# Kernel optimization log

Measured on AMD Instinct MI355X. Metric: run time of the kernel, lower is better.

## Reference

```python
import jax, jax.numpy as jnp
import numpy as np

B, N, F, P, HID, OUT = 4, 20000, 8, 12, 64, 1
E = 320000


def _glorot(k, shape):
    lim = float(np.sqrt(6.0 / (shape[0] + shape[1])))
    return jax.random.uniform(k, shape, jnp.float32, -lim, lim)


def setup_inputs() -> dict:
    key = jax.random.key(0)
    ks = jax.random.split(key, 20)
    inp = {
        "x": jax.random.normal(ks[0], (B, N, F, P), jnp.float32),
        "edge_index": jax.random.randint(ks[1], (2, E), 0, N, jnp.int64),
        "edge_attr": jax.random.uniform(ks[2], (E,), jnp.float32),
        # GCNConv weights (stored [in, out]) + biases for z, r, h gates
        "conv_z_w": _glorot(ks[3], (F, HID)), "conv_z_b": jnp.zeros((HID,), jnp.float32),
        "conv_r_w": _glorot(ks[4], (F, HID)), "conv_r_b": jnp.zeros((HID,), jnp.float32),
        "conv_h_w": _glorot(ks[5], (F, HID)), "conv_h_b": jnp.zeros((HID,), jnp.float32),
        # GRU linear layers on cat([conv_out, H]) -> HID (stored [in, out])
        "lin_z_w": _glorot(ks[6], (2 * HID, HID)), "lin_z_b": jnp.zeros((HID,), jnp.float32),
        "lin_r_w": _glorot(ks[7], (2 * HID, HID)), "lin_r_b": jnp.zeros((HID,), jnp.float32),
        "lin_h_w": _glorot(ks[8], (2 * HID, HID)), "lin_h_b": jnp.zeros((HID,), jnp.float32),
        # temporal attention logits over periods
        "attention": jax.random.uniform(ks[9], (P,), jnp.float32),
        # final linear: HID -> OUT*P
        "out_w": _glorot(ks[10], (HID, OUT * P)), "out_b": jnp.zeros((OUT * P,), jnp.float32),
    }
    return inp


def reference(x, edge_index, edge_attr,
              conv_z_w, conv_z_b, conv_r_w, conv_r_b, conv_h_w, conv_h_b,
              lin_z_w, lin_z_b, lin_r_w, lin_r_b, lin_h_w, lin_h_b,
              attention, out_w, out_b):
    Bb, Nn, Ff, Pp = x.shape
    Hh = conv_z_w.shape[1]

    # GCN normalization with self loops: A_hat = D^-1/2 (A + I) D^-1/2
    loop = jnp.arange(Nn)
    row = jnp.concatenate([edge_index[0], loop])
    col = jnp.concatenate([edge_index[1], loop])
    w = jnp.concatenate([edge_attr, jnp.ones((Nn,), x.dtype)])
    deg = jax.ops.segment_sum(w, col, num_segments=Nn)
    dinv = jnp.where(deg > 0, jax.lax.rsqrt(deg), 0.0)
    norm = dinv[row] * w * dinv[col]  # [E+N]

    def gcn(xt, W, b):
        # xt: [B, N, F] -> [B, N, H]
        xw = jnp.einsum('bnf,fh->bnh', xt, W)
        msg = xw[:, row, :] * norm[None, :, None]            # gather over source nodes
        agg = jax.vmap(lambda m: jax.ops.segment_sum(m, col, num_segments=Nn))(msg)
        return agg + b

    H0 = jnp.zeros((Bb, Nn, Hh), x.dtype)  # A3TGCN2 passes H=None each period -> zeros

    def tgcn_cell(xt):
        Z = jax.nn.sigmoid(jnp.concatenate([gcn(xt, conv_z_w, conv_z_b), H0], -1) @ lin_z_w + lin_z_b)
        R = jax.nn.sigmoid(jnp.concatenate([gcn(xt, conv_r_w, conv_r_b), H0], -1) @ lin_r_w + lin_r_b)
        Ht = jnp.tanh(jnp.concatenate([gcn(xt, conv_h_w, conv_h_b), H0 * R], -1) @ lin_h_w + lin_h_b)
        return Z * H0 + (1.0 - Z) * Ht

    probs = jax.nn.softmax(attention)
    xs = jnp.moveaxis(x, -1, 0)  # [P, B, N, F]

    def step(acc, inp):
        xt, p = inp
        return acc + p * tgcn_cell(xt), None

    h_accum, _ = jax.lax.scan(step, jnp.zeros((Bb, Nn, Hh), x.dtype), (xs, probs))

    h = jax.nn.relu(h_accum)
    out = h @ out_w + out_b                 # [B, N, OUT*P]
    return out.reshape(Bb, Nn, -1, Pp)      # [B, N, OUT, P]
```

## Files before the change

### kernel.cpp

```cpp
#include <hip/hip_runtime.h>

#define NN 20000
#define EE 320000
#define NPB 8
#define CAP 64
#define LCAP 80
#define OVCAP 8192

#define WZ_O 0
#define BZ_O 512
#define WH_O 576
#define BH_O 1088
#define OW_O 1152
#define OB_O 1920
#define PR_O 1932
#define NCONST 1944

__device__ __forceinline__ float b2f(unsigned short h) {
  union { unsigned int u; float f; } v; v.u = ((unsigned int)h) << 16; return v.f;
}
__device__ __forceinline__ unsigned short f2b(float f) {
  union { unsigned int u; float f; } v; v.f = f;
  unsigned int u = v.u;
  unsigned int r = (u + 0x7fffu + ((u >> 16) & 1u)) >> 16;
  return (unsigned short)r;
}
__device__ __forceinline__ float ldw(const void* p, int i, int isbf) {
  return isbf ? b2f(((const unsigned short*)p)[i]) : ((const float*)p)[i];
}
__device__ __forceinline__ void upk(unsigned int w, float& x0, float& x1) {
  union { unsigned int u; float f; } lo, hi;
  lo.u = w << 16; hi.u = w & 0xffff0000u;
  x0 = lo.f; x1 = hi.f;
}
__device__ __forceinline__ float degf(unsigned long long dc) {
  return (float)(unsigned int)dc * (1.0f / 1048576.0f);
}

__global__ void k_init(const unsigned int* __restrict__ ei_w,
                       const unsigned int* __restrict__ ea_w,
                       int* __restrict__ flags,
                       unsigned long long* __restrict__ degcnt,
                       int* __restrict__ ovf_cnt,
                       float* __restrict__ consts,
                       const void* czw, const void* czb,
                       const void* chw, const void* chb,
                       const void* lzw, const void* lzb,
                       const void* lhw, const void* lhb,
                       const void* att, const void* ow, const void* ob) {
  int tid = threadIdx.x;
  int i = blockIdx.x * 256 + tid;
  if (i < NN) degcnt[i] = 0ull;
  if (blockIdx.x == 1 && tid == 0) *ovf_cnt = 0;
  if (blockIdx.x != 0) return;

  __shared__ int sfl[2];
  if (tid < 64) {
    unsigned long long b1 = __ballot((ea_w[tid] >> 15) & 1u);
    unsigned long long b2 = __ballot(ei_w[2 * tid + 1] != 0u);
    if (tid == 0) {
      int f0 = (b1 == 0ull) ? 1 : 0;
      int f1 = (b2 == 0ull) ? 1 : 0;
      flags[0] = f0; flags[1] = f1; sfl[0] = f0; sfl[1] = f1;
    }
  }
  __syncthreads();
  int isbf = sfl[0];

  for (int idx = tid; idx < 512; idx += 256) {
    int f = idx >> 6, k = idx & 63;
    float sz = 0.f, sh = 0.f;
    for (int h = 0; h < 64; ++h) {
      sz += ldw(czw, f * 64 + h, isbf) * ldw(lzw, h * 64 + k, isbf);
      sh += ldw(chw, f * 64 + h, isbf) * ldw(lhw, h * 64 + k, isbf);
    }
    consts[WZ_O + idx] = sz; consts[WH_O + idx] = sh;
  }
  for (int idx = tid; idx < 64; idx += 256) {
    float sz = ldw(lzb, idx, isbf), sh = ldw(lhb, idx, isbf);
    for (int h = 0; h < 64; ++h) {
      sz += ldw(czb, h, isbf) * ldw(lzw, h * 64 + idx, isbf);
      sh += ldw(chb, h, isbf) * ldw(lhw, h * 64 + idx, isbf);
    }
    consts[BZ_O + idx] = sz; consts[BH_O + idx] = sh;
  }
  for (int idx = tid; idx < 768; idx += 256) consts[OW_O + idx] = ldw(ow, idx, isbf);
  if (tid < 12) consts[OB_O + tid] = ldw(ob, tid, isbf);
  if (tid == 0) {
    float a[12]; float m = -1e30f;
    for (int p = 0; p < 12; ++p) { a[p] = ldw(att, p, isbf); m = fmaxf(m, a[p]); }
    float ssum = 0.f;
    for (int p = 0; p < 12; ++p) { a[p] = __expf(a[p] - m); ssum += a[p]; }
    for (int p = 0; p < 12; ++p) consts[PR_O + p] = a[p] / ssum;
  }
}

__global__ void k_append(const void* __restrict__ ei, const void* __restrict__ ea,
                         const int* __restrict__ flags,
                         unsigned long long* __restrict__ degcnt,
                         unsigned int* __restrict__ slab,
                         int* __restrict__ ovf_cnt, int* __restrict__ ovf_dst,
                         unsigned int* __restrict__ ovf_pack) {
  int isbf = flags[0], is64 = flags[1];
  int e = blockIdx.x * blockDim.x + threadIdx.x;
  if (e >= EE) return;
  int r, c;
  if (is64) {
    r = (int)((const unsigned int*)ei)[2 * e];
    c = (int)((const unsigned int*)ei)[2 * (EE + e)];
  } else {
    r = ((const int*)ei)[e];
    c = ((const int*)ei)[EE + e];
  }
  unsigned short wb;
  float w;
  if (isbf) { wb = ((const unsigned short*)ea)[e]; w = b2f(wb); }
  else      { w = ((const float*)ea)[e]; wb = f2b(w); }
  unsigned long long pk = (1ull << 32) |
      (unsigned long long)(unsigned int)__float2int_rn(w * 1048576.0f);
  unsigned long long old = atomicAdd(&degcnt[c], pk);
  int pos = (int)(old >> 32);
  unsigned int packed = ((unsigned int)wb << 16) | (unsigned int)r;
  if (pos < CAP) {
    slab[c * CAP + pos] = packed;
  } else {
    int oi = atomicAdd(ovf_cnt, 1);
    if (oi < OVCAP) { ovf_dst[oi] = c; ovf_pack[oi] = packed; }
  }
}

__global__ void __launch_bounds__(192) k_node(
    const void* __restrict__ x,
    const unsigned long long* __restrict__ degcnt,
    const unsigned int* __restrict__ slab,
    const int* __restrict__ ovf_cnt, const int* __restrict__ ovf_dst,
    const unsigned int* __restrict__ ovf_pack,
    const float* __restrict__ consts, const int* __restrict__ flags,
    void* __restrict__ out) {
  __shared__ __align__(16) float sc[792];
  __shared__ __align__(16) float pacc[4 * 384];
  __shared__ __align__(16) float acc[384];
  __shared__ __align__(16) float hpart[768];
  __shared__ __align__(16) float hfin[256];
  __shared__ int   sedge[NPB * LCAP];
  __shared__ float vedge[NPB * LCAP];
  __shared__ int   scnt[NPB];
  __shared__ float sdn[NPB];

  const int tid = threadIdx.x;
  const int isbf = flags[0];
  const int n0 = blockIdx.x * NPB;

  for (int i = tid; i < 792; i += 192) sc[i] = consts[OW_O + i];

  const int g  = tid / 48;
  const int c  = tid % 48;
  const int k  = tid & 63;
  const int g3 = tid >> 6;
  const int bc = c / 12;
  const int oc = 8 * (c % 12);
  const long xoff = (long)bc * (NN * 96) + oc;

  float wz[8], wh[8];
#pragma unroll
  for (int f = 0; f < 8; ++f) {
    wz[f] = consts[WZ_O + f * 64 + k];
    wh[f] = consts[WH_O + f * 64 + k];
  }
  const float bz = consts[BZ_O + k], bh = consts[BH_O + k];

  if (tid < NPB) {
    unsigned long long dc = degcnt[n0 + tid];
    int cnt = (int)(dc >> 32);
    scnt[tid] = cnt < CAP ? cnt : CAP;
    sdn[tid] = rsqrtf(degf(dc) + 1.0f);
  }
  __syncthreads();

  for (int i = tid; i < NPB * CAP; i += 192) {
    int ni = i >> 6, slot = i & (CAP - 1);
    int cnt = (int)(degcnt[n0 + ni] >> 32);
    if (cnt > CAP) cnt = CAP;
    if (slot < cnt) {
      unsigned int pk = slab[(n0 + ni) * CAP + slot];
      int s = (int)(pk & 0xffffu);
      float w = b2f((unsigned short)(pk >> 16));
      sedge[ni * LCAP + slot] = s * 96;
      vedge[ni * LCAP + slot] = w * rsqrtf(degf(degcnt[s]) + 1.0f);
    }
  }
  {
    int ov = ovf_cnt[0];
    if (ov > 0) {
      if (ov > OVCAP) ov = OVCAP;
      for (int i = tid; i < ov; i += 192) {
        unsigned int dd = (unsigned int)(ovf_dst[i] - n0);
        if (dd < NPB) {
          int idx = atomicAdd(&scnt[dd], 1);
          if (idx < LCAP) {
            unsigned int pk = ovf_pack[i];
            int s = (int)(pk & 0xffffu);
            float w = b2f((unsigned short)(pk >> 16));
            sedge[dd * LCAP + idx] = s * 96;
            vedge[dd * LCAP + idx] = w * rsqrtf(degf(degcnt[s]) + 1.0f);
          }
        }
      }
    }
  }
  __syncthreads();

  for (int ni = 0; ni < NPB; ++ni) {
    const int n = n0 + ni;
    int m = scnt[ni]; if (m > LCAP) m = LCAP;
    const float dn = sdn[ni];
    float a[8];
#pragma unroll
    for (int t = 0; t < 8; ++t) a[t] = 0.f;

    if (isbf) {
      const unsigned short* xb = (const unsigned short*)x;
      for (int j = g; j < m; j += 4) {
        int soff = sedge[ni * LCAP + j];
        float v = vedge[ni * LCAP + j];
        uint4 u = *(const uint4*)(xb + xoff + soff);
        float x0, x1;
        upk(u.x, x0, x1); a[0] += v * x0; a[1] += v * x1;
        upk(u.y, x0, x1); a[2] += v * x0; a[3] += v * x1;
        upk(u.z, x0, x1); a[4] += v * x0; a[5] += v * x1;
        upk(u.w, x0, x1); a[6] += v * x0; a[7] += v * x1;
      }
      if (g == 0) {
        uint4 u = *(const uint4*)(xb + xoff + (long)n * 96);
        float x0, x1;
        upk(u.x, x0, x1); a[0] += dn * x0; a[1] += dn * x1;
        upk(u.y, x0, x1); a[2] += dn * x0; a[3] += dn * x1;
        upk(u.z, x0, x1); a[4] += dn * x0; a[5] += dn * x1;
        upk(u.w, x0, x1); a[6] += dn * x0; a[7] += dn * x1;
      }
    } else {
      const float* xf = (const float*)x;
      for (int j = g; j < m; j += 4) {
        int soff = sedge[ni * LCAP + j];
        float v = vedge[ni * LCAP + j];
        const float4* px = (const float4*)(xf + xoff + soff);
        float4 u0 = px[0], u1 = px[1];
        a[0] += v * u0.x; a[1] += v * u0.y; a[2] += v * u0.z; a[3] += v * u0.w;
        a[4] += v * u1.x; a[5] += v * u1.y; a[6] += v * u1.z; a[7] += v * u1.w;
      }
      if (g == 0) {
        const float4* px = (const float4*)(xf + xoff + (long)n * 96);
        float4 u0 = px[0], u1 = px[1];
        a[0] += dn * u0.x; a[1] += dn * u0.y; a[2] += dn * u0.z; a[3] += dn * u0.w;
        a[4] += dn * u1.x; a[5] += dn * u1.y; a[6] += dn * u1.z; a[7] += dn * u1.w;
      }
    }
    {
      float4* pg = (float4*)&pacc[g * 384 + 8 * c];
      pg[0] = make_float4(a[0], a[1], a[2], a[3]);
      pg[1] = make_float4(a[4], a[5], a[6], a[7]);
    }
    __syncthreads();
    for (int i = tid; i < 384; i += 192) {
      int b = i / 96, r = i % 96, p = r >> 3, f = r & 7;
      int src = b * 96 + f * 12 + p;
      acc[i] = dn * (pacc[src] + pacc[384 + src] + pacc[768 + src] + pacc[1152 + src]);
    }
    __syncthreads();

    float hb0 = 0.f, hb1 = 0.f, hb2 = 0.f, hb3 = 0.f;
#pragma unroll
    for (int pi = 0; pi < 4; ++pi) {
      int p = g3 + 3 * pi;
      float pr = sc[780 + p];
#pragma unroll
      for (int b = 0; b < 4; ++b) {
        const float4* A = (const float4*)&acc[b * 96 + p * 8];
        float4 A0 = A[0], A1 = A[1];
        float za = bz + A0.x * wz[0] + A0.y * wz[1] + A0.z * wz[2] + A0.w * wz[3]
                      + A1.x * wz[4] + A1.y * wz[5] + A1.z * wz[6] + A1.w * wz[7];
        float ta = bh + A0.x * wh[0] + A0.y * wh[1] + A0.z * wh[2] + A0.w * wh[3]
                      + A1.x * wh[4] + A1.y * wh[5] + A1.z * wh[6] + A1.w * wh[7];
        float ea = __expf(za);
        float eh = __expf(2.0f * fminf(ta, 40.0f));
        float cc = pr * (eh - 1.0f) * __builtin_amdgcn_rcpf((1.0f + ea) * (1.0f + eh));
        if (b == 0) hb0 += cc; else if (b == 1) hb1 += cc;
        else if (b == 2) hb2 += cc; else hb3 += cc;
      }
    }
    hpart[g3 * 256 +   0 + k] = hb0;
    hpart[g3 * 256 +  64 + k] = hb1;
    hpart[g3 * 256 + 128 + k] = hb2;
    hpart[g3 * 256 + 192 + k] = hb3;
    __syncthreads();
    for (int i = tid; i < 256; i += 192)
      hfin[i] = fmaxf(hpart[i] + hpart[256 + i] + hpart[512 + i], 0.f);
    __syncthreads();

    if (tid < 48) {
      int b = tid / 12, p = tid % 12;
      float o = sc[768 + p];
#pragma unroll 8
      for (int k2 = 0; k2 < 64; ++k2) o += hfin[b * 64 + k2] * sc[k2 * 12 + p];
      int oi = (b * NN + n) * 12 + p;
      if (isbf) ((unsigned short*)out)[oi] = f2b(o);
      else      ((float*)out)[oi] = o;
    }
  }
}

extern "C" void kernel_launch(void* const* d_in, const int* in_sizes, int n_in,
                              void* d_out, int out_size, void* d_ws, size_t ws_size,
                              hipStream_t stream) {
  const void* x   = d_in[0];
  const void* ei  = d_in[1];
  const void* ea  = d_in[2];
  const void* czw = d_in[3];
  const void* czb = d_in[4];
  const void* chw = d_in[7];
  const void* chb = d_in[8];
  const void* lzw = d_in[9];
  const void* lzb = d_in[10];
  const void* lhw = d_in[13];
  const void* lhb = d_in[14];
  const void* att = d_in[15];
  const void* ow  = d_in[16];
  const void* ob  = d_in[17];

  char* ws = (char*)d_ws;
  int*   flags   = (int*)  (ws + 0);
  float* consts  = (float*)(ws + 256);
  unsigned long long* degcnt = (unsigned long long*)(ws + 8192);
  int*   ovf_cnt = (int*)  (ws + 168192);
  int*   ovf_dst = (int*)  (ws + 168448);
  unsigned int* ovf_pack = (unsigned int*)(ws + 201216);
  unsigned int* slab     = (unsigned int*)(ws + 240000);

  k_init<<<dim3(79), dim3(256), 0, stream>>>((const unsigned int*)ei,
                                             (const unsigned int*)ea, flags, degcnt,
                                             ovf_cnt, consts, czw, czb, chw, chb,
                                             lzw, lzb, lhw, lhb, att, ow, ob);
  k_append<<<dim3(1250), dim3(256), 0, stream>>>(ei, ea, flags, degcnt, slab,
                                                 ovf_cnt, ovf_dst, ovf_pack);
  k_node<<<dim3(NN / NPB), dim3(192), 0, stream>>>(x, degcnt, slab, ovf_cnt, ovf_dst,
                                                   ovf_pack, consts, flags, d_out);
}
```

Measured before the change: 260.2 us.

## Split node kernel across batch dimension with 16-way edge parallelism

Launches the node kernel with one block per (batch, node-group), so each block handles a single batch element and splits edges 16 ways instead of 4. The reduction, gate computation and output projection are reshaped to per-batch sizes, and the output dot product uses shuffle-based partial sums. This raises parallelism and cuts per-thread serial edge work. In exchange, the per-block edge list setup, degree loads and weight loads are now repeated four times.

Result: slower. 292.4 us (+12.4%).

```diff
diff --git a/kernel.cpp b/kernel.cpp
--- a/kernel.cpp
+++ b/kernel.cpp
@@ -3,9 +3,11 @@
 #define NN 20000
 #define EE 320000
 #define NPB 8
+#define NBLK 2500
 #define CAP 64
 #define LCAP 80
 #define OVCAP 8192
+#define PROW 104
 
 #define WZ_O 0
 #define BZ_O 512
@@ -137,29 +139,28 @@
     const unsigned int* __restrict__ ovf_pack,
     const float* __restrict__ consts, const int* __restrict__ flags,
     void* __restrict__ out) {
-  __shared__ __align__(16) float sc[792];
-  __shared__ __align__(16) float pacc[4 * 384];
-  __shared__ __align__(16) float acc[384];
-  __shared__ __align__(16) float hpart[768];
-  __shared__ __align__(16) float hfin[256];
+  __shared__ __align__(16) float sow[792];
+  __shared__ __align__(16) float pacc[16 * PROW];
+  __shared__ __align__(16) float accT[96];
+  __shared__ __align__(16) float hpart[192];
   __shared__ int   sedge[NPB * LCAP];
   __shared__ float vedge[NPB * LCAP];
   __shared__ int   scnt[NPB];
   __shared__ float sdn[NPB];
 
-  const int tid = threadIdx.x;
+  const int tid  = threadIdx.x;
   const int isbf = flags[0];
-  const int n0 = blockIdx.x * NPB;
-
-  for (int i = tid; i < 792; i += 192) sc[i] = consts[OW_O + i];
-
-  const int g  = tid / 48;
-  const int c  = tid % 48;
-  const int k  = tid & 63;
-  const int g3 = tid >> 6;
-  const int bc = c / 12;
-  const int oc = 8 * (c % 12);
-  const long xoff = (long)bc * (NN * 96) + oc;
+  const int bb   = blockIdx.x / NBLK;
+  const int n0   = (blockIdx.x % NBLK) * NPB;
+
+  for (int i = tid; i < 792; i += 192) sow[i] = consts[OW_O + i];
+
+  const int sub = tid / 12;
+  const int q   = tid % 12;
+  const int k   = tid & 63;
+  const int g3  = tid / 64;
+
+  const long xbase = (long)bb * (NN * 96) + 8 * q;
 
   float wz[8], wh[8];
 #pragma unroll
@@ -220,18 +221,18 @@
 
     if (isbf) {
       const unsigned short* xb = (const unsigned short*)x;
-      for (int j = g; j < m; j += 4) {
+      for (int j = sub; j < m; j += 16) {
         int soff = sedge[ni * LCAP + j];
         float v = vedge[ni * LCAP + j];
-        uint4 u = *(const uint4*)(xb + xoff + soff);
+        uint4 u = *(const uint4*)(xb + xbase + soff);
         float x0, x1;
         upk(u.x, x0, x1); a[0] += v * x0; a[1] += v * x1;
         upk(u.y, x0, x1); a[2] += v * x0; a[3] += v * x1;
         upk(u.z, x0, x1); a[4] += v * x0; a[5] += v * x1;
         upk(u.w, x0, x1); a[6] += v * x0; a[7] += v * x1;
       }
-      if (g == 0) {
-        uint4 u = *(const uint4*)(xb + xoff + (long)n * 96);
+      if (sub == 0) {
+        uint4 u = *(const uint4*)(xb + xbase + (long)n * 96);
         float x0, x1;
         upk(u.x, x0, x1); a[0] += dn * x0; a[1] += dn * x1;
         upk(u.y, x0, x1); a[2] += dn * x0; a[3] += dn * x1;
@@ -240,71 +241,73 @@
       }
     } else {
       const float* xf = (const float*)x;
-      for (int j = g; j < m; j += 4) {
+      for (int j = sub; j < m; j += 16) {
         int soff = sedge[ni * LCAP + j];
         float v = vedge[ni * LCAP + j];
-        const float4* px = (const float4*)(xf + xoff + soff);
+        const float4* px = (const float4*)(xf + xbase + soff);
         float4 u0 = px[0], u1 = px[1];
         a[0] += v * u0.x; a[1] += v * u0.y; a[2] += v * u0.z; a[3] += v * u0.w;
         a[4] += v * u1.x; a[5] += v * u1.y; a[6] += v * u1.z; a[7] += v * u1.w;
       }
-      if (g == 0) {
-        const float4* px = (const float4*)(xf + xoff + (long)n * 96);
+      if (sub == 0) {
+        const float4* px = (const float4*)(xf + xbase + (long)n * 96);
         float4 u0 = px[0], u1 = px[1];
         a[0] += dn * u0.x; a[1] += dn * u0.y; a[2] += dn * u0.z; a[3] += dn * u0.w;
         a[4] += dn * u1.x; a[5] += dn * u1.y; a[6] += dn * u1.z; a[7] += dn * u1.w;
       }
     }
     {
-      float4* pg = (float4*)&pacc[g * 384 + 8 * c];
+      float4* pg = (float4*)&pacc[sub * PROW + 8 * q];
       pg[0] = make_float4(a[0], a[1], a[2], a[3]);
       pg[1] = make_float4(a[4], a[5], a[6], a[7]);
     }
     __syncthreads();
-    for (int i = tid; i < 384; i += 192) {
-      int b = i / 96, r = i % 96, p = r >> 3, f = r & 7;
-      int src = b * 96 + f * 12 + p;
-      acc[i] = dn * (pacc[src] + pacc[384 + src] + pacc[768 + src] + pacc[1152 + src]);
+    if (tid < 96) {
+      int p = tid >> 3, f = tid & 7;
+      int src = f * 12 + p;
+      float s0 = 0.f;
+#pragma unroll
+      for (int s = 0; s < 16; ++s) s0 += pacc[s * PROW + src];
+      accT[tid] = dn * s0;
     }
     __syncthreads();
 
-    float hb0 = 0.f, hb1 = 0.f, hb2 = 0.f, hb3 = 0.f;
+    float hb = 0.f;
 #pragma unroll
     for (int pi = 0; pi < 4; ++pi) {
       int p = g3 + 3 * pi;
-      float pr = sc[780 + p];
-#pragma unroll
-      for (int b = 0; b < 4; ++b) {
-        const float4* A = (const float4*)&acc[b * 96 + p * 8];
-        float4 A0 = A[0], A1 = A[1];
-        float za = bz + A0.x * wz[0] + A0.y * wz[1] + A0.z * wz[2] + A0.w * wz[3]
-                      + A1.x * wz[4] + A1.y * wz[5] + A1.z * wz[6] + A1.w * wz[7];
-        float ta = bh + A0.x * wh[0] + A0.y * wh[1] + A0.z * wh[2] + A0.w * wh[3]
-                      + A1.x * wh[4] + A1.y * wh[5] + A1.z * wh[6] + A1.w * wh[7];
-        float ea = __expf(za);
-        float eh = __expf(2.0f * fminf(ta, 40.0f));
-        float cc = pr * (eh - 1.0f) * __builtin_amdgcn_rcpf((1.0f + ea) * (1.0f + eh));
-        if (b == 0) hb0 += cc; else if (b == 1) hb1 += cc;
-        else if (b == 2) hb2 += cc; else hb3 += cc;
-      }
-    }
-    hpart[g3 * 256 +   0 + k] = hb0;
-    hpart[g3 * 256 +  64 + k] = hb1;
-    hpart[g3 * 256 + 128 + k] = hb2;
-    hpart[g3 * 256 + 192 + k] = hb3;
+      float pr = sow[780 + p];
+      const float4* A = (const float4*)&accT[p * 8];
+      float4 A0 = A[0], A1 = A[1];
+      float za = bz + A0.x * wz[0] + A0.y * wz[1] + A0.z * wz[2] + A0.w * wz[3]
+                    + A1.x * wz[4] + A1.y * wz[5] + A1.z * wz[6] + A1.w * wz[7];
+      float ta = bh + A0.x * wh[0] + A0.y * wh[1] + A0.z * wh[2] + A0.w * wh[3]
+                    + A1.x * wh[4] + A1.y * wh[5] + A1.z * wh[6] + A1.w * wh[7];
+      float ea = __expf(za);
+      float eh = __expf(2.0f * fminf(ta, 40.0f));
+      hb += pr * (eh - 1.0f) * __builtin_amdgcn_rcpf((1.0f + ea) * (1.0f + eh));
+    }
+    hpart[g3 * 64 + k] = hb;
     __syncthreads();
-    for (int i = tid; i < 256; i += 192)
-      hfin[i] = fmaxf(hpart[i] + hpart[256 + i] + hpart[512 + i], 0.f);
-    __syncthreads();
-
-    if (tid < 48) {
-      int b = tid / 12, p = tid % 12;
-      float o = sc[768 + p];
-#pragma unroll 8
-      for (int k2 = 0; k2 < 64; ++k2) o += hfin[b * 64 + k2] * sc[k2 * 12 + p];
-      int oi = (b * NN + n) * 12 + p;
-      if (isbf) ((unsigned short*)out)[oi] = f2b(o);
-      else      ((float*)out)[oi] = o;
+
+    if (tid < 96) {
+      int p = tid >> 3, kq = tid & 7;
+      float o = 0.f;
+#pragma unroll
+      for (int j = 0; j < 8; ++j) {
+        int kk = kq * 8 + j;
+        float h = fmaxf(hpart[kk] + hpart[64 + kk] + hpart[128 + kk], 0.f);
+        o += h * sow[kk * 12 + p];
+      }
+      o += __shfl_xor(o, 1);
+      o += __shfl_xor(o, 2);
+      o += __shfl_xor(o, 4);
+      if (kq == 0) {
+        float oo = o + sow[768 + p];
+        int oi = (bb * NN + n) * 12 + p;
+        if (isbf) ((unsigned short*)out)[oi] = f2b(oo);
+        else      ((float*)out)[oi] = oo;
+      }
     }
   }
 }
@@ -342,6 +345,6 @@
                                              lzw, lzb, lhw, lhb, att, ow, ob);
   k_append<<<dim3(1250), dim3(256), 0, stream>>>(ei, ea, flags, degcnt, slab,
                                                  ovf_cnt, ovf_dst, ovf_pack);
-  k_node<<<dim3(NN / NPB), dim3(192), 0, stream>>>(x, degcnt, slab, ovf_cnt, ovf_dst,
+  k_node<<<dim3(4 * NBLK), dim3(192), 0, stream>>>(x, degcnt, slab, ovf_cnt, ovf_dst,
                                                    ovf_pack, consts, flags, d_out);
 }
```

## Map one wavefront per node in k_node, removing block-wide syncs per node

Applied to the files above, without the earlier changes.

Restructures k_node so each 64-lane wavefront handles one node (4 nodes per 256-thread block) instead of a 192-thread block looping over 8 nodes with several __syncthreads per node. Each wave gathers its own edge list, including the self-loop as an extra entry, and accumulates with 2-way unrolled loads. It then computes the gates over all 12 periods per lane and does the output projection against a transposed, padded out_w held in shared memory. Only wave barriers are used after the setup. This removes block-level synchronisation and the cross-group partial-sum reductions, but only 48 of 64 lanes do the gather and each lane walks the whole edge list serially.

New measurement: 240.4 us. 7.6% less time.

```diff
diff --git a/kernel.cpp b/kernel.cpp
--- a/kernel.cpp
+++ b/kernel.cpp
@@ -2,19 +2,18 @@
 
 #define NN 20000
 #define EE 320000
-#define NPB 8
 #define CAP 64
-#define LCAP 80
+#define SVC 72
 #define OVCAP 8192
 
 #define WZ_O 0
 #define BZ_O 512
 #define WH_O 576
 #define BH_O 1088
-#define OW_O 1152
-#define OB_O 1920
-#define PR_O 1932
-#define NCONST 1944
+#define OWT_O 1152
+#define OB_O 1968
+#define PR_O 1980
+#define NCONST 1992
 
 __device__ __forceinline__ float b2f(unsigned short h) {
   union { unsigned int u; float f; } v; v.u = ((unsigned int)h) << 16; return v.f;
@@ -84,7 +83,10 @@
     }
     consts[BZ_O + idx] = sz; consts[BH_O + idx] = sh;
   }
-  for (int idx = tid; idx < 768; idx += 256) consts[OW_O + idx] = ldw(ow, idx, isbf);
+  for (int idx = tid; idx < 816; idx += 256) {
+    int p = idx / 68, kk = idx % 68;
+    consts[OWT_O + idx] = (kk < 64) ? ldw(ow, kk * 12 + p, isbf) : 0.f;
+  }
   if (tid < 12) consts[OB_O + tid] = ldw(ob, tid, isbf);
   if (tid == 0) {
     float a[12]; float m = -1e30f;
@@ -129,7 +131,19 @@
   }
 }
 
-__global__ void __launch_bounds__(192) k_node(
+#define ACC8(u, v)                                           \
+  { float x0, x1;                                            \
+    upk((u).x, x0, x1); a[0] += (v) * x0; a[1] += (v) * x1;  \
+    upk((u).y, x0, x1); a[2] += (v) * x0; a[3] += (v) * x1;  \
+    upk((u).z, x0, x1); a[4] += (v) * x0; a[5] += (v) * x1;  \
+    upk((u).w, x0, x1); a[6] += (v) * x0; a[7] += (v) * x1; }
+
+#define ACCF8(u0, u1, v)                                                       \
+  { a[0] += (v) * (u0).x; a[1] += (v) * (u0).y; a[2] += (v) * (u0).z;          \
+    a[3] += (v) * (u0).w; a[4] += (v) * (u1).x; a[5] += (v) * (u1).y;          \
+    a[6] += (v) * (u1).z; a[7] += (v) * (u1).w; }
+
+__global__ void __launch_bounds__(256) k_node(
     const void* __restrict__ x,
     const unsigned long long* __restrict__ degcnt,
     const unsigned int* __restrict__ slab,
@@ -137,145 +151,124 @@
     const unsigned int* __restrict__ ovf_pack,
     const float* __restrict__ consts, const int* __restrict__ flags,
     void* __restrict__ out) {
-  __shared__ __align__(16) float sc[792];
-  __shared__ __align__(16) float pacc[4 * 384];
-  __shared__ __align__(16) float acc[384];
-  __shared__ __align__(16) float hpart[768];
-  __shared__ __align__(16) float hfin[256];
-  __shared__ int   sedge[NPB * LCAP];
-  __shared__ float vedge[NPB * LCAP];
-  __shared__ int   scnt[NPB];
-  __shared__ float sdn[NPB];
-
-  const int tid = threadIdx.x;
+  __shared__ __align__(16) float sow[840];
+  __shared__ __align__(16) int2  sv[4 * SVC];
+  __shared__ __align__(16) float accT[4 * 384];
+  __shared__ __align__(16) float hw[4 * 272];
+  __shared__ int swcnt[4];
+
+  const int tid  = threadIdx.x;
+  const int w    = tid >> 6;
+  const int lane = tid & 63;
   const int isbf = flags[0];
-  const int n0 = blockIdx.x * NPB;
-
-  for (int i = tid; i < 792; i += 192) sc[i] = consts[OW_O + i];
-
-  const int g  = tid / 48;
-  const int c  = tid % 48;
-  const int k  = tid & 63;
-  const int g3 = tid >> 6;
-  const int bc = c / 12;
-  const int oc = 8 * (c % 12);
-  const long xoff = (long)bc * (NN * 96) + oc;
-
+  const int n    = blockIdx.x * 4 + w;
+
+  for (int i = tid; i < 840; i += 256) sow[i] = consts[OWT_O + i];
   float wz[8], wh[8];
 #pragma unroll
   for (int f = 0; f < 8; ++f) {
-    wz[f] = consts[WZ_O + f * 64 + k];
-    wh[f] = consts[WH_O + f * 64 + k];
-  }
-  const float bz = consts[BZ_O + k], bh = consts[BH_O + k];
-
-  if (tid < NPB) {
-    unsigned long long dc = degcnt[n0 + tid];
-    int cnt = (int)(dc >> 32);
-    scnt[tid] = cnt < CAP ? cnt : CAP;
-    sdn[tid] = rsqrtf(degf(dc) + 1.0f);
-  }
-  __syncthreads();
-
-  for (int i = tid; i < NPB * CAP; i += 192) {
-    int ni = i >> 6, slot = i & (CAP - 1);
-    int cnt = (int)(degcnt[n0 + ni] >> 32);
-    if (cnt > CAP) cnt = CAP;
-    if (slot < cnt) {
-      unsigned int pk = slab[(n0 + ni) * CAP + slot];
-      int s = (int)(pk & 0xffffu);
-      float w = b2f((unsigned short)(pk >> 16));
-      sedge[ni * LCAP + slot] = s * 96;
-      vedge[ni * LCAP + slot] = w * rsqrtf(degf(degcnt[s]) + 1.0f);
-    }
-  }
+    wz[f] = consts[WZ_O + f * 64 + lane];
+    wh[f] = consts[WH_O + f * 64 + lane];
+  }
+  const float bz = consts[BZ_O + lane], bh = consts[BH_O + lane];
+
+  unsigned long long dcn = degcnt[n];
+  int cnt = (int)(dcn >> 32);
+  int base = cnt < CAP ? cnt : CAP;
+  const float dn = rsqrtf(degf(dcn) + 1.0f);
+  int2* svw = &sv[w * SVC];
+  if (lane == 0) swcnt[w] = base;
+  if (lane < base) {
+    unsigned int pk = slab[n * CAP + lane];
+    int s = (int)(pk & 0xffffu);
+    float v = b2f((unsigned short)(pk >> 16)) * rsqrtf(degf(degcnt[s]) + 1.0f);
+    svw[lane] = make_int2(s * 96, __float_as_int(v));
+  }
+  int m0 = base;
   {
     int ov = ovf_cnt[0];
     if (ov > 0) {
       if (ov > OVCAP) ov = OVCAP;
-      for (int i = tid; i < ov; i += 192) {
-        unsigned int dd = (unsigned int)(ovf_dst[i] - n0);
-        if (dd < NPB) {
-          int idx = atomicAdd(&scnt[dd], 1);
-          if (idx < LCAP) {
+      for (int i = lane; i < ov; i += 64) {
+        if (ovf_dst[i] == n) {
+          int idx = atomicAdd(&swcnt[w], 1);
+          if (idx < SVC - 1) {
             unsigned int pk = ovf_pack[i];
             int s = (int)(pk & 0xffffu);
-            float w = b2f((unsigned short)(pk >> 16));
-            sedge[dd * LCAP + idx] = s * 96;
-            vedge[dd * LCAP + idx] = w * rsqrtf(degf(degcnt[s]) + 1.0f);
+            float v = b2f((unsigned short)(pk >> 16)) * rsqrtf(degf(degcnt[s]) + 1.0f);
+            svw[idx] = make_int2(s * 96, __float_as_int(v));
           }
         }
       }
-    }
-  }
+      __builtin_amdgcn_wave_barrier();
+      m0 = swcnt[w];
+      if (m0 > SVC - 1) m0 = SVC - 1;
+    }
+  }
+  if (lane == 0) svw[m0] = make_int2(n * 96, __float_as_int(dn));
+  const int m1 = m0 + 1;
   __syncthreads();
 
-  for (int ni = 0; ni < NPB; ++ni) {
-    const int n = n0 + ni;
-    int m = scnt[ni]; if (m > LCAP) m = LCAP;
-    const float dn = sdn[ni];
-    float a[8];
-#pragma unroll
-    for (int t = 0; t < 8; ++t) a[t] = 0.f;
-
+  float a[8];
+#pragma unroll
+  for (int t = 0; t < 8; ++t) a[t] = 0.f;
+  if (lane < 48) {
+    const long xbase = (long)(lane / 12) * (NN * 96) + 8 * (lane % 12);
     if (isbf) {
       const unsigned short* xb = (const unsigned short*)x;
-      for (int j = g; j < m; j += 4) {
-        int soff = sedge[ni * LCAP + j];
-        float v = vedge[ni * LCAP + j];
-        uint4 u = *(const uint4*)(xb + xoff + soff);
-        float x0, x1;
-        upk(u.x, x0, x1); a[0] += v * x0; a[1] += v * x1;
-        upk(u.y, x0, x1); a[2] += v * x0; a[3] += v * x1;
-        upk(u.z, x0, x1); a[4] += v * x0; a[5] += v * x1;
-        upk(u.w, x0, x1); a[6] += v * x0; a[7] += v * x1;
-      }
-      if (g == 0) {
-        uint4 u = *(const uint4*)(xb + xoff + (long)n * 96);
-        float x0, x1;
-        upk(u.x, x0, x1); a[0] += dn * x0; a[1] += dn * x1;
-        upk(u.y, x0, x1); a[2] += dn * x0; a[3] += dn * x1;
-        upk(u.z, x0, x1); a[4] += dn * x0; a[5] += dn * x1;
-        upk(u.w, x0, x1); a[6] += dn * x0; a[7] += dn * x1;
+      int j = 0;
+      for (; j + 1 < m1; j += 2) {
+        int2 e0 = svw[j], e1 = svw[j + 1];
+        uint4 u0 = *(const uint4*)(xb + xbase + e0.x);
+        uint4 u1 = *(const uint4*)(xb + xbase + e1.x);
+        float v0 = __int_as_float(e0.y), v1 = __int_as_float(e1.y);
+        ACC8(u0, v0); ACC8(u1, v1);
+      }
+      if (j < m1) {
+        int2 e0 = svw[j];
+        uint4 u0 = *(const uint4*)(xb + xbase + e0.x);
+        float v0 = __int_as_float(e0.y);
+        ACC8(u0, v0);
       }
     } else {
       const float* xf = (const float*)x;
-      for (int j = g; j < m; j += 4) {
-        int soff = sedge[ni * LCAP + j];
-        float v = vedge[ni * LCAP + j];
-        const float4* px = (const float4*)(xf + xoff + soff);
-        float4 u0 = px[0], u1 = px[1];
-        a[0] += v * u0.x; a[1] += v * u0.y; a[2] += v * u0.z; a[3] += v * u0.w;
-        a[4] += v * u1.x; a[5] += v * u1.y; a[6] += v * u1.z; a[7] += v * u1.w;
-      }
-      if (g == 0) {
-        const float4* px = (const float4*)(xf + xoff + (long)n * 96);
-        float4 u0 = px[0], u1 = px[1];
-        a[0] += dn * u0.x; a[1] += dn * u0.y; a[2] += dn * u0.z; a[3] += dn * u0.w;
-        a[4] += dn * u1.x; a[5] += dn * u1.y; a[6] += dn * u1.z; a[7] += dn * u1.w;
-      }
-    }
-    {
-      float4* pg = (float4*)&pacc[g * 384 + 8 * c];
-      pg[0] = make_float4(a[0], a[1], a[2], a[3]);
-      pg[1] = make_float4(a[4], a[5], a[6], a[7]);
-    }
-    __syncthreads();
-    for (int i = tid; i < 384; i += 192) {
-      int b = i / 96, r = i % 96, p = r >> 3, f = r & 7;
-      int src = b * 96 + f * 12 + p;
-      acc[i] = dn * (pacc[src] + pacc[384 + src] + pacc[768 + src] + pacc[1152 + src]);
-    }
-    __syncthreads();
-
-    float hb0 = 0.f, hb1 = 0.f, hb2 = 0.f, hb3 = 0.f;
-#pragma unroll
-    for (int pi = 0; pi < 4; ++pi) {
-      int p = g3 + 3 * pi;
-      float pr = sc[780 + p];
-#pragma unroll
-      for (int b = 0; b < 4; ++b) {
-        const float4* A = (const float4*)&acc[b * 96 + p * 8];
+      int j = 0;
+      for (; j + 1 < m1; j += 2) {
+        int2 e0 = svw[j], e1 = svw[j + 1];
+        const float4* p0 = (const float4*)(xf + xbase + e0.x);
+        const float4* p1 = (const float4*)(xf + xbase + e1.x);
+        float4 u00 = p0[0], u01 = p0[1], u10 = p1[0], u11 = p1[1];
+        float v0 = __int_as_float(e0.y), v1 = __int_as_float(e1.y);
+        ACCF8(u00, u01, v0); ACCF8(u10, u11, v1);
+      }
+      if (j < m1) {
+        int2 e0 = svw[j];
+        const float4* p0 = (const float4*)(xf + xbase + e0.x);
+        float4 u00 = p0[0], u01 = p0[1];
+        float v0 = __int_as_float(e0.y);
+        ACCF8(u00, u01, v0);
+      }
+    }
+    float* accTw = &accT[w * 384];
+    const int bq = (lane / 12) * 96, oc = 8 * (lane % 12);
+#pragma unroll
+    for (int t = 0; t < 8; ++t) {
+      int eib = oc + t;
+      int f = eib / 12, p = eib % 12;
+      accTw[bq + p * 8 + f] = dn * a[t];
+    }
+  }
+  __builtin_amdgcn_wave_barrier();
+
+  {
+    const float* accTw = &accT[w * 384];
+    float* hww = &hw[w * 272];
+#pragma unroll
+    for (int b = 0; b < 4; ++b) {
+      float hbl = 0.f;
+#pragma unroll
+      for (int p = 0; p < 12; ++p) {
+        const float4* A = (const float4*)&accTw[b * 96 + p * 8];
         float4 A0 = A[0], A1 = A[1];
         float za = bz + A0.x * wz[0] + A0.y * wz[1] + A0.z * wz[2] + A0.w * wz[3]
                       + A1.x * wz[4] + A1.y * wz[5] + A1.z * wz[6] + A1.w * wz[7];
@@ -283,29 +276,27 @@
                       + A1.x * wh[4] + A1.y * wh[5] + A1.z * wh[6] + A1.w * wh[7];
         float ea = __expf(za);
         float eh = __expf(2.0f * fminf(ta, 40.0f));
-        float cc = pr * (eh - 1.0f) * __builtin_amdgcn_rcpf((1.0f + ea) * (1.0f + eh));
-        if (b == 0) hb0 += cc; else if (b == 1) hb1 += cc;
-        else if (b == 2) hb2 += cc; else hb3 += cc;
-      }
-    }
-    hpart[g3 * 256 +   0 + k] = hb0;
-    hpart[g3 * 256 +  64 + k] = hb1;
-    hpart[g3 * 256 + 128 + k] = hb2;
-    hpart[g3 * 256 + 192 + k] = hb3;
-    __syncthreads();
-    for (int i = tid; i < 256; i += 192)
-      hfin[i] = fmaxf(hpart[i] + hpart[256 + i] + hpart[512 + i], 0.f);
-    __syncthreads();
-
-    if (tid < 48) {
-      int b = tid / 12, p = tid % 12;
-      float o = sc[768 + p];
-#pragma unroll 8
-      for (int k2 = 0; k2 < 64; ++k2) o += hfin[b * 64 + k2] * sc[k2 * 12 + p];
-      int oi = (b * NN + n) * 12 + p;
-      if (isbf) ((unsigned short*)out)[oi] = f2b(o);
-      else      ((float*)out)[oi] = o;
-    }
+        hbl += sow[828 + p] * (eh - 1.0f) *
+               __builtin_amdgcn_rcpf((1.0f + ea) * (1.0f + eh));
+      }
+      hww[b * 68 + lane] = fmaxf(hbl, 0.f);
+    }
+  }
+  __builtin_amdgcn_wave_barrier();
+
+  if (lane < 48) {
+    const float* hww = &hw[w * 272];
+    int b = lane / 12, p = lane % 12;
+    float o = sow[816 + p];
+#pragma unroll
+    for (int kq = 0; kq < 16; ++kq) {
+      float4 hv = *(const float4*)&hww[b * 68 + 4 * kq];
+      float4 wv = *(const float4*)&sow[p * 68 + 4 * kq];
+      o += hv.x * wv.x + hv.y * wv.y + hv.z * wv.z + hv.w * wv.w;
+    }
+    int oi = (b * NN + n) * 12 + p;
+    if (isbf) ((unsigned short*)out)[oi] = f2b(o);
+    else      ((float*)out)[oi] = o;
   }
 }
 
@@ -330,10 +321,10 @@
   char* ws = (char*)d_ws;
   int*   flags   = (int*)  (ws + 0);
   float* consts  = (float*)(ws + 256);
-  unsigned long long* degcnt = (unsigned long long*)(ws + 8192);
-  int*   ovf_cnt = (int*)  (ws + 168192);
-  int*   ovf_dst = (int*)  (ws + 168448);
-  unsigned int* ovf_pack = (unsigned int*)(ws + 201216);
+  unsigned long long* degcnt = (unsigned long long*)(ws + 8448);
+  int*   ovf_cnt = (int*)  (ws + 168448);
+  int*   ovf_dst = (int*)  (ws + 168704);
+  unsigned int* ovf_pack = (unsigned int*)(ws + 201472);
   unsigned int* slab     = (unsigned int*)(ws + 240000);
 
   k_init<<<dim3(79), dim3(256), 0, stream>>>((const unsigned int*)ei,
@@ -342,6 +333,6 @@
                                              lzw, lzb, lhw, lhb, att, ow, ob);
   k_append<<<dim3(1250), dim3(256), 0, stream>>>(ei, ea, flags, degcnt, slab,
                                                  ovf_cnt, ovf_dst, ovf_pack);
-  k_node<<<dim3(NN / NPB), dim3(192), 0, stream>>>(x, degcnt, slab, ovf_cnt, ovf_dst,
-                                                   ovf_pack, consts, flags, d_out);
-}
+  k_node<<<dim3(NN / 4), dim3(256), 0, stream>>>(x, degcnt, slab, ovf_cnt, ovf_dst,
+                                                 ovf_pack, consts, flags, d_out);
+}
```
